# Kernel tuning notes

Hardware: AMD Instinct MI355X
Metric: run time of the kernel (lower is better)

The kernel has to match this reference:

```python
import jax, jax.numpy as jnp
import numpy as np

N, E, G, L, H, DIN = 50000, 800000, 500, 4, 64, 128
EPS = 1e-5


def _gcn(x, W, b, src, dst, n):
    h = x @ W
    loop = jnp.arange(n)
    s = jnp.concatenate([src, loop])
    d = jnp.concatenate([dst, loop])
    deg = jax.ops.segment_sum(jnp.ones(s.shape[0], x.dtype), d, num_segments=n)
    dinv = jax.lax.rsqrt(jnp.maximum(deg, 1.0))  # deg >= 1 due to self loops
    norm = (dinv[s] * dinv[d])[:, None]
    return jax.ops.segment_sum(h[s] * norm, d, num_segments=n) + b


def _g2(x, W, b, src, dst, n, p=2.0):
    # G2 gradient gate: tau = tanh(scatter_mean_over_src(|X_src - X_dst|^p))
    Xc = jax.nn.relu(_gcn(x, W, b, src, dst, n))
    diff = jnp.abs(Xc[src] - Xc[dst]) ** p  # [E, H]
    s = jax.ops.segment_sum(diff, src, num_segments=n)
    cnt = jax.ops.segment_sum(jnp.ones(src.shape[0], x.dtype), src, num_segments=n)
    return jnp.tanh(s / jnp.maximum(cnt, 1.0)[:, None])


def _bn(x, g, b):
    # BatchNorm1d with batch statistics (training-mode normalization)
    m = x.mean(0)
    v = x.var(0)
    return (x - m) * jax.lax.rsqrt(v + EPS) * g + b


def setup_inputs() -> dict:
    key = jax.random.key(0)
    ks = jax.random.split(key, 24)
    sc_in = 1.0 / np.sqrt(DIN)
    sc_h = 1.0 / np.sqrt(H)
    inp = {
        "x": jax.random.normal(ks[0], (N, DIN), jnp.float32),
        "edge_index": jax.random.randint(ks[1], (2, E), 0, N),
        "batch": jnp.sort(jax.random.randint(ks[2], (N,), 0, G)),
        "preW": jax.random.normal(ks[3], (DIN, H), jnp.float32) * sc_in,
        "preb": jnp.zeros((H,), jnp.float32),
        "convW": jax.random.normal(ks[4], (L, H, H), jnp.float32) * sc_h,
        "convb": jnp.zeros((L, H), jnp.float32),
        "ggW": jax.random.normal(ks[5], (L, H, H), jnp.float32) * sc_h,
        "ggb": jnp.zeros((L, H), jnp.float32),
        "lin1W": jax.random.normal(ks[6], (H, H), jnp.float32) * sc_h,
        "lin1b": jnp.zeros((H,), jnp.float32),
        "lin2W": jax.random.normal(ks[7], (H, H), jnp.float32) * sc_h,
        "lin2b": jnp.zeros((H,), jnp.float32),
        "lin3W": jax.random.normal(ks[8], (H, H), jnp.float32) * sc_h,
        "lin3b": jnp.zeros((H,), jnp.float32),
        "lin4W": jax.random.normal(ks[9], (H, 1), jnp.float32) * sc_h,
        "lin4b": jnp.zeros((1,), jnp.float32),
        "bn_g": jnp.ones((H,), jnp.float32),
        "bn_b": jnp.zeros((H,), jnp.float32),
    }
    return inp


def reference(x, edge_index, batch, preW, preb, convW, convb, ggW, ggb,
              lin1W, lin1b, lin2W, lin2b, lin3W, lin3b, lin4W, lin4b,
              bn_g, bn_b):
    src, dst = edge_index[0], edge_index[1]
    # prelinear (dropout disabled / eval)
    x = jax.nn.relu(x @ preW + preb)
    for l in range(L):
        x_ = jax.nn.relu(_gcn(x, convW[l], convb[l], src, dst, N))
        tau = _g2(x, ggW[l], ggb[l], src, dst, N)
        x = (1.0 - tau) * x + tau * x_
    # readout: global add pool per graph -> [G, H]
    h = jax.ops.segment_sum(x, batch, num_segments=G)
    out = jax.nn.relu(_bn(h @ lin1W + lin1b, bn_g, bn_b))
    out = jax.nn.relu(_bn(out @ lin2W + lin2b, bn_g, bn_b))
    out = jax.nn.relu(_bn(out @ lin3W + lin3b, bn_g, bn_b))
    out = out @ lin4W + lin4b  # [G, 1]
    energy = 0.5 * jnp.sum((x[src] - x[dst]) ** 2)  # dirichlet energy of final x
    return (out, out, energy)
```

## Files before the change

kernel.cpp:

```cpp
#include <hip/hip_runtime.h>
#include <hip/hip_bf16.h>


#define N_NODES 50000
#define N_EDGES 800000
#define N_GRAPH 500
#define N_LAYERS 4
#define HDIM 64
#define DDIN 128
#define BN_EPS 1e-5f
#define NEPART 256
#define SC_CHUNK 2048
#define SC_NBLK ((N_NODES + SC_CHUNK - 1) / SC_CHUNK)
#define NPARTS 8
#define PRNG (N_NODES / NPARTS)
#define FILL_BPP 56

typedef __hip_bfloat16 bf16;


__global__ __launch_bounds__(256) void k_degrees(const int* __restrict__ ei,
                                                 int* __restrict__ deg_in,
                                                 int* __restrict__ deg_out) {
  int part = blockIdx.x & (NPARTS - 1);
  int slice = blockIdx.x >> 3;
  int nslice = gridDim.x >> 3;
  int lo = part * PRNG, hi = lo + PRNG;
  int stride = nslice * 256;
  for (int e = slice * 256 + threadIdx.x; e < N_EDGES; e += stride) {
    int s = ei[e], d = ei[N_EDGES + e];
    if (s >= lo && s < hi) atomicAdd(&deg_out[s], 1);
    if (d >= lo && d < hi) atomicAdd(&deg_in[d], 1);
  }
}

__global__ __launch_bounds__(256) void k_scan1(const int* __restrict__ deg_in,
                                               const int* __restrict__ deg_out,
                                               int* __restrict__ rp_dst,
                                               int* __restrict__ rp_src,
                                               int* __restrict__ bsum) {
  int arr = blockIdx.y;
  const int* in = arr ? deg_out : deg_in;
  int* out = arr ? rp_src : rp_dst;
  int base = blockIdx.x * SC_CHUNK + threadIdx.x * 8;
  int v[8];
  int s = 0;
#pragma unroll
  for (int j = 0; j < 8; ++j) {
    int ii = base + j;
    v[j] = (ii < N_NODES) ? in[ii] : 0;
    s += v[j];
  }
  __shared__ int sh[256];
  sh[threadIdx.x] = s;
  __syncthreads();
  for (int off = 1; off < 256; off <<= 1) {
    int t = (threadIdx.x >= off) ? sh[threadIdx.x - off] : 0;
    __syncthreads();
    sh[threadIdx.x] += t;
    __syncthreads();
  }
  int run = sh[threadIdx.x] - s;
#pragma unroll
  for (int j = 0; j < 8; ++j) {
    int ii = base + j;
    if (ii < N_NODES) out[ii] = run;
    run += v[j];
  }
  if (threadIdx.x == 255) bsum[arr * SC_NBLK + blockIdx.x] = sh[255];
}

__global__ __launch_bounds__(64) void k_scan2(const int* __restrict__ bsum,
                                              int* __restrict__ boff,
                                              int* __restrict__ rp_dst,
                                              int* __restrict__ rp_src) {
  int lane = threadIdx.x;
  for (int a = 0; a < 2; ++a) {
    int v = (lane < SC_NBLK) ? bsum[a * SC_NBLK + lane] : 0;
    int incl = v;
    for (int off = 1; off < 64; off <<= 1) {
      int t = __shfl_up(incl, off);
      if (lane >= off) incl += t;
    }
    if (lane < SC_NBLK) boff[a * SC_NBLK + lane] = incl - v;
  }
  if (lane == 0) {
    rp_dst[N_NODES] = N_EDGES;
    rp_src[N_NODES] = N_EDGES;
  }
}

__global__ __launch_bounds__(256) void k_scan3(const int* __restrict__ boff,
                                               int* __restrict__ rp_dst,
                                               int* __restrict__ rp_src,
                                               int* __restrict__ cur_dst,
                                               int* __restrict__ cur_src,
                                               const int* __restrict__ deg_in,
                                               float* __restrict__ dinv) {
  int arr = blockIdx.y;
  int* rp = arr ? rp_src : rp_dst;
  int* cur = arr ? cur_src : cur_dst;
  int off = boff[arr * SC_NBLK + blockIdx.x];
  int base = blockIdx.x * SC_CHUNK + threadIdx.x * 8;
#pragma unroll
  for (int j = 0; j < 8; ++j) {
    int ii = base + j;
    if (ii < N_NODES) {
      int v = rp[ii] + off;
      rp[ii] = v;
      cur[ii] = v;
      if (arr == 0) dinv[ii] = rsqrtf((float)(deg_in[ii] + 1));
    }
  }
}

__global__ __launch_bounds__(256) void k_fill(const int* __restrict__ ei,
                                              int* __restrict__ cur_dst,
                                              int* __restrict__ cur_src,
                                              int* __restrict__ csr_dst,
                                              int* __restrict__ csr_src) {
  int part = blockIdx.x & (NPARTS - 1);
  int slice = blockIdx.x >> 3;
  int nslice = gridDim.x >> 3;
  int lo = part * PRNG, hi = lo + PRNG;
  int stride = nslice * 256;
  for (int e = slice * 256 + threadIdx.x; e < N_EDGES; e += stride) {
    int s = ei[e], d = ei[N_EDGES + e];
    if (d >= lo && d < hi) {
      int q = atomicAdd(&cur_dst[d], 1);
      csr_dst[q] = s;
    }
    if (s >= lo && s < hi) {
      int q = atomicAdd(&cur_src[s], 1);
      csr_src[q] = d;
    }
  }
}


__global__ __launch_bounds__(256) void k_prelin(const float* __restrict__ x0,
                                                const float* __restrict__ W,
                                                const float* __restrict__ b,
                                                float* __restrict__ x) {
  __shared__ float Ws[DDIN * HDIM];
  for (int t = threadIdx.x; t < DDIN * HDIM; t += 256) Ws[t] = W[t];
  __syncthreads();
  int wave = threadIdx.x >> 6, lane = threadIdx.x & 63;
  float bias = b[lane];
  int stride = gridDim.x * 4;
  for (int i = blockIdx.x * 4 + wave; i < N_NODES; i += stride) {
    const float* xr = x0 + (size_t)i * DDIN;
    float xl0 = xr[lane], xl1 = xr[64 + lane];
    float acc = bias;
#pragma unroll
    for (int k = 0; k < 64; ++k) acc = fmaf(__shfl(xl0, k), Ws[k * 64 + lane], acc);
#pragma unroll
    for (int k = 0; k < 64; ++k) acc = fmaf(__shfl(xl1, k), Ws[(64 + k) * 64 + lane], acc);
    x[(size_t)i * HDIM + lane] = fmaxf(acc, 0.f);
  }
}

__global__ __launch_bounds__(256) void k_agg(const float* __restrict__ x,
                                             const int* __restrict__ rp,
                                             const int* __restrict__ csr,
                                             const float* __restrict__ dinv,
                                             float* __restrict__ aggb) {
  int i = (blockIdx.x * 256 + threadIdx.x) >> 6;
  int lane = threadIdx.x & 63;
  if (i >= N_NODES) return;
  int e0 = rp[i], e1 = rp[i + 1];
  float di = dinv[i];
  size_t li = (size_t)i * HDIM + lane;
  float a0 = x[li] * di, a1 = 0.f, a2 = 0.f, a3 = 0.f;
  for (int base = e0; base < e1; base += 64) {
    int m = e1 - base;
    if (m > 64) m = 64;
    int idx = csr[base + (lane < m ? lane : 0)];
    float dv = dinv[idx];
    int k = 0;
    for (; k + 8 <= m; k += 8) {
      int s0 = __shfl(idx, k), s1 = __shfl(idx, k + 1), s2 = __shfl(idx, k + 2),
          s3 = __shfl(idx, k + 3), s4 = __shfl(idx, k + 4), s5 = __shfl(idx, k + 5),
          s6 = __shfl(idx, k + 6), s7 = __shfl(idx, k + 7);
      float w0 = __shfl(dv, k), w1 = __shfl(dv, k + 1), w2 = __shfl(dv, k + 2),
            w3 = __shfl(dv, k + 3), w4 = __shfl(dv, k + 4), w5 = __shfl(dv, k + 5),
            w6 = __shfl(dv, k + 6), w7 = __shfl(dv, k + 7);
      float v0 = x[(size_t)s0 * HDIM + lane], v1 = x[(size_t)s1 * HDIM + lane];
      float v2 = x[(size_t)s2 * HDIM + lane], v3 = x[(size_t)s3 * HDIM + lane];
      float v4 = x[(size_t)s4 * HDIM + lane], v5 = x[(size_t)s5 * HDIM + lane];
      float v6 = x[(size_t)s6 * HDIM + lane], v7 = x[(size_t)s7 * HDIM + lane];
      a0 = fmaf(v0, w0, a0);
      a1 = fmaf(v1, w1, a1);
      a2 = fmaf(v2, w2, a2);
      a3 = fmaf(v3, w3, a3);
      a0 = fmaf(v4, w4, a0);
      a1 = fmaf(v5, w5, a1);
      a2 = fmaf(v6, w6, a2);
      a3 = fmaf(v7, w7, a3);
    }
    for (; k < m; ++k) {
      int s = __shfl(idx, k);
      float w = __shfl(dv, k);
      a0 = fmaf(x[(size_t)s * HDIM + lane], w, a0);
    }
  }
  aggb[li] = (a0 + a1 + a2 + a3) * di;
}

__global__ __launch_bounds__(256) void k_gemm2(const float* __restrict__ agg,
                                               const float* __restrict__ W1,
                                               const float* __restrict__ W2,
                                               const float* __restrict__ b1,
                                               const float* __restrict__ b2,
                                               float* __restrict__ x_,
                                               bf16* __restrict__ Xch) {
  __shared__ float W1s[HDIM * HDIM], W2s[HDIM * HDIM];
  for (int t = threadIdx.x; t < HDIM * HDIM; t += 256) {
    W1s[t] = W1[t];
    W2s[t] = W2[t];
  }
  __syncthreads();
  int wave = threadIdx.x >> 6, lane = threadIdx.x & 63;
  float bb1 = b1[lane], bb2 = b2[lane];
  int stride = gridDim.x * 4;
  for (int i = blockIdx.x * 4 + wave; i < N_NODES; i += stride) {
    size_t li = (size_t)i * HDIM + lane;
    float xl = agg[li];
    float r1 = 0.f, r2 = 0.f;
#pragma unroll
    for (int k = 0; k < 64; ++k) {
      float xv = __shfl(xl, k);
      r1 = fmaf(xv, W1s[k * 64 + lane], r1);
      r2 = fmaf(xv, W2s[k * 64 + lane], r2);
    }
    x_[li] = fmaxf(r1 + bb1, 0.f);
    Xch[li] = __float2bfloat16(fmaxf(r2 + bb2, 0.f));
  }
}

__global__ __launch_bounds__(256) void k_gate(const bf16* __restrict__ Xch,
                                              const float* __restrict__ x_,
                                              const int* __restrict__ rp,
                                              const int* __restrict__ csr,
                                              float* __restrict__ x,
                                              bf16* __restrict__ xh) {
  int i = (blockIdx.x * 256 + threadIdx.x) >> 6;
  int lane = threadIdx.x & 63;
  if (i >= N_NODES) return;
  int e0 = rp[i], e1 = rp[i + 1];
  float xi = __bfloat162float(Xch[(size_t)i * HDIM + lane]);
  float a0 = 0.f, a1 = 0.f, a2 = 0.f, a3 = 0.f;
  for (int base = e0; base < e1; base += 64) {
    int m = e1 - base;
    if (m > 64) m = 64;
    int idx = csr[base + (lane < m ? lane : 0)];
    int k = 0;
    for (; k + 8 <= m; k += 8) {
      int s0 = __shfl(idx, k), s1 = __shfl(idx, k + 1), s2 = __shfl(idx, k + 2),
          s3 = __shfl(idx, k + 3), s4 = __shfl(idx, k + 4), s5 = __shfl(idx, k + 5),
          s6 = __shfl(idx, k + 6), s7 = __shfl(idx, k + 7);
      float v0 = __bfloat162float(Xch[(size_t)s0 * HDIM + lane]);
      float v1 = __bfloat162float(Xch[(size_t)s1 * HDIM + lane]);
      float v2 = __bfloat162float(Xch[(size_t)s2 * HDIM + lane]);
      float v3 = __bfloat162float(Xch[(size_t)s3 * HDIM + lane]);
      float v4 = __bfloat162float(Xch[(size_t)s4 * HDIM + lane]);
      float v5 = __bfloat162float(Xch[(size_t)s5 * HDIM + lane]);
      float v6 = __bfloat162float(Xch[(size_t)s6 * HDIM + lane]);
      float v7 = __bfloat162float(Xch[(size_t)s7 * HDIM + lane]);
      float t0 = xi - v0, t1 = xi - v1, t2 = xi - v2, t3 = xi - v3;
      float t4 = xi - v4, t5 = xi - v5, t6 = xi - v6, t7 = xi - v7;
      a0 = fmaf(t0, t0, a0);
      a1 = fmaf(t1, t1, a1);
      a2 = fmaf(t2, t2, a2);
      a3 = fmaf(t3, t3, a3);
      a0 = fmaf(t4, t4, a0);
      a1 = fmaf(t5, t5, a1);
      a2 = fmaf(t6, t6, a2);
      a3 = fmaf(t7, t7, a3);
    }
    for (; k < m; ++k) {
      int d = __shfl(idx, k);
      float t = xi - __bfloat162float(Xch[(size_t)d * HDIM + lane]);
      a0 = fmaf(t, t, a0);
    }
  }
  int cnt = e1 - e0;
  float tau = tanhf((a0 + a1 + a2 + a3) / (float)(cnt > 0 ? cnt : 1));
  size_t idx = (size_t)i * HDIM + lane;
  float xn = (1.f - tau) * x[idx] + tau * x_[idx];
  x[idx] = xn;
  xh[idx] = __float2bfloat16(xn);
}

__global__ __launch_bounds__(256) void k_epool(const float* __restrict__ x,
                                               const bf16* __restrict__ xh,
                                               const int* __restrict__ rp,
                                               const int* __restrict__ csr,
                                               const int* __restrict__ batch,
                                               float* __restrict__ hpool,
                                               float* __restrict__ epart) {
  int i = (blockIdx.x * 256 + threadIdx.x) >> 6;
  int lane = threadIdx.x & 63;
  if (i >= N_NODES) return;
  size_t li = (size_t)i * HDIM + lane;
  float xi = __bfloat162float(xh[li]);
  int e0 = rp[i], e1 = rp[i + 1];
  float a0 = 0.f, a1 = 0.f, a2 = 0.f, a3 = 0.f;
  for (int base = e0; base < e1; base += 64) {
    int m = e1 - base;
    if (m > 64) m = 64;
    int idx = csr[base + (lane < m ? lane : 0)];
    int k = 0;
    for (; k + 8 <= m; k += 8) {
      int s0 = __shfl(idx, k), s1 = __shfl(idx, k + 1), s2 = __shfl(idx, k + 2),
          s3 = __shfl(idx, k + 3), s4 = __shfl(idx, k + 4), s5 = __shfl(idx, k + 5),
          s6 = __shfl(idx, k + 6), s7 = __shfl(idx, k + 7);
      float v0 = __bfloat162float(xh[(size_t)s0 * HDIM + lane]);
      float v1 = __bfloat162float(xh[(size_t)s1 * HDIM + lane]);
      float v2 = __bfloat162float(xh[(size_t)s2 * HDIM + lane]);
      float v3 = __bfloat162float(xh[(size_t)s3 * HDIM + lane]);
      float v4 = __bfloat162float(xh[(size_t)s4 * HDIM + lane]);
      float v5 = __bfloat162float(xh[(size_t)s5 * HDIM + lane]);
      float v6 = __bfloat162float(xh[(size_t)s6 * HDIM + lane]);
      float v7 = __bfloat162float(xh[(size_t)s7 * HDIM + lane]);
      float t0 = xi - v0, t1 = xi - v1, t2 = xi - v2, t3 = xi - v3;
      float t4 = xi - v4, t5 = xi - v5, t6 = xi - v6, t7 = xi - v7;
      a0 = fmaf(t0, t0, a0);
      a1 = fmaf(t1, t1, a1);
      a2 = fmaf(t2, t2, a2);
      a3 = fmaf(t3, t3, a3);
      a0 = fmaf(t4, t4, a0);
      a1 = fmaf(t5, t5, a1);
      a2 = fmaf(t6, t6, a2);
      a3 = fmaf(t7, t7, a3);
    }
    for (; k < m; ++k) {
      int d = __shfl(idx, k);
      float t = xi - __bfloat162float(xh[(size_t)d * HDIM + lane]);
      a0 = fmaf(t, t, a0);
    }
  }
  int g = batch[i];
  atomicAdd(&hpool[g * HDIM + lane], x[li]);
  float acc = a0 + a1 + a2 + a3;
  acc += __shfl_down(acc, 32);
  acc += __shfl_down(acc, 16);
  acc += __shfl_down(acc, 8);
  acc += __shfl_down(acc, 4);
  acc += __shfl_down(acc, 2);
  acc += __shfl_down(acc, 1);
  if (lane == 0) atomicAdd(&epart[i & (NEPART - 1)], acc);
}

__global__ __launch_bounds__(256) void k_esum(const float* __restrict__ epart,
                                              float* __restrict__ out_e) {
  __shared__ float sh[NEPART];
  int t = threadIdx.x;
  sh[t] = epart[t];
  __syncthreads();
  for (int off = NEPART / 2; off > 0; off >>= 1) {
    if (t < off) sh[t] += sh[t + off];
    __syncthreads();
  }
  if (t == 0) out_e[0] = 0.5f * sh[0];
}


__global__ __launch_bounds__(256) void k_mlpbn(const float* __restrict__ Hin,
                                               const float* __restrict__ W,
                                               const float* __restrict__ b,
                                               const float* __restrict__ g,
                                               const float* __restrict__ bb,
                                               float* __restrict__ Z) {
  int c = blockIdx.x;
  __shared__ float Wc[HDIM];
  __shared__ float red[256];
  if (threadIdx.x < HDIM) Wc[threadIdx.x] = W[threadIdx.x * HDIM + c];
  __syncthreads();
  int r0 = threadIdx.x, r1 = threadIdx.x + 256;
  float bc = b[c];
  float d0 = bc, d1 = bc;
  if (r0 < N_GRAPH) {
    const float* h = Hin + (size_t)r0 * HDIM;
#pragma unroll
    for (int k = 0; k < HDIM; ++k) d0 = fmaf(h[k], Wc[k], d0);
  }
  if (r1 < N_GRAPH) {
    const float* h = Hin + (size_t)r1 * HDIM;
#pragma unroll
    for (int k = 0; k < HDIM; ++k) d1 = fmaf(h[k], Wc[k], d1);
  }
  red[threadIdx.x] = (r0 < N_GRAPH ? d0 : 0.f) + (r1 < N_GRAPH ? d1 : 0.f);
  __syncthreads();
  for (int off = 128; off > 0; off >>= 1) {
    if (threadIdx.x < off) red[threadIdx.x] += red[threadIdx.x + off];
    __syncthreads();
  }
  float mean = red[0] / (float)N_GRAPH;
  __syncthreads();
  float t0 = (r0 < N_GRAPH) ? d0 - mean : 0.f;
  float t1 = (r1 < N_GRAPH) ? d1 - mean : 0.f;
  red[threadIdx.x] = t0 * t0 + t1 * t1;
  __syncthreads();
  for (int off = 128; off > 0; off >>= 1) {
    if (threadIdx.x < off) red[threadIdx.x] += red[threadIdx.x + off];
    __syncthreads();
  }
  float var = red[0] / (float)N_GRAPH;
  float scale = rsqrtf(var + BN_EPS) * g[c];
  float bias = bb[c];
  if (r0 < N_GRAPH) Z[(size_t)r0 * HDIM + c] = fmaxf(fmaf(t0, scale, bias), 0.f);
  if (r1 < N_GRAPH) Z[(size_t)r1 * HDIM + c] = fmaxf(fmaf(t1, scale, bias), 0.f);
}

__global__ __launch_bounds__(256) void k_final(const float* __restrict__ H,
                                               const float* __restrict__ w,
                                               const float* __restrict__ b,
                                               float* __restrict__ out) {
  int r = blockIdx.x * 256 + threadIdx.x;
  if (r >= N_GRAPH) return;
  float acc = b[0];
#pragma unroll
  for (int k = 0; k < 64; ++k) acc = fmaf(H[r * HDIM + k], w[k], acc);
  out[r] = acc;
  out[N_GRAPH + r] = acc;
}


extern "C" void kernel_launch(void* const* d_in, const int* in_sizes, int n_in,
                              void* d_out, int out_size, void* d_ws, size_t ws_size,
                              hipStream_t stream) {
  (void)in_sizes; (void)n_in; (void)out_size; (void)ws_size;
  const float* x0    = (const float*)d_in[0];
  const int*   ei    = (const int*)d_in[1];
  const int*   batch = (const int*)d_in[2];
  const float* preW  = (const float*)d_in[3];
  const float* preb  = (const float*)d_in[4];
  const float* convW = (const float*)d_in[5];
  const float* convb = (const float*)d_in[6];
  const float* ggW   = (const float*)d_in[7];
  const float* ggb   = (const float*)d_in[8];
  const float* lin1W = (const float*)d_in[9];
  const float* lin1b = (const float*)d_in[10];
  const float* lin2W = (const float*)d_in[11];
  const float* lin2b = (const float*)d_in[12];
  const float* lin3W = (const float*)d_in[13];
  const float* lin3b = (const float*)d_in[14];
  const float* lin4W = (const float*)d_in[15];
  const float* lin4b = (const float*)d_in[16];
  const float* bng   = (const float*)d_in[17];
  const float* bnb   = (const float*)d_in[18];
  float* out = (float*)d_out;

  char* ws = (char*)d_ws;
  size_t off = 0;
  auto alloc = [&](size_t bytes) -> void* {
    off = (off + 255) & ~(size_t)255;
    void* p = ws + off;
    off += bytes;
    return p;
  };
  int* deg_in   = (int*)alloc(2ull * N_NODES * 4);
  int* deg_out  = deg_in + N_NODES;
  int* rp_dst   = (int*)alloc((N_NODES + 1) * 4);
  int* rp_src   = (int*)alloc((N_NODES + 1) * 4);
  int* cur_dst  = (int*)alloc((N_NODES + 1) * 4);
  int* cur_src  = (int*)alloc((N_NODES + 1) * 4);
  int* bsum     = (int*)alloc(2 * SC_NBLK * 4);
  int* boff     = (int*)alloc(2 * SC_NBLK * 4);
  int* csr_dst  = (int*)alloc((size_t)N_EDGES * 4);
  int* csr_src  = (int*)alloc((size_t)N_EDGES * 4);
  float* dinv   = (float*)alloc(N_NODES * 4);
  float* x      = (float*)alloc((size_t)N_NODES * HDIM * 4);
  float* aggb   = (float*)alloc((size_t)N_NODES * HDIM * 4);
  float* x_     = (float*)alloc((size_t)N_NODES * HDIM * 4);
  bf16* Xch     = (bf16*)alloc((size_t)N_NODES * HDIM * 2);
  bf16* xh      = (bf16*)alloc((size_t)N_NODES * HDIM * 2);
  float* hpool  = (float*)alloc(N_GRAPH * HDIM * 4);
  float* epart  = (float*)alloc(NEPART * 4);
  float* mlpA   = (float*)alloc(N_GRAPH * HDIM * 4);
  float* mlpB   = (float*)alloc(N_GRAPH * HDIM * 4);

  hipMemsetAsync(deg_in, 0, 2ull * N_NODES * 4, stream);
  hipMemsetAsync(hpool, 0, N_GRAPH * HDIM * 4, stream);
  hipMemsetAsync(epart, 0, NEPART * 4, stream);

  k_degrees<<<NPARTS * FILL_BPP, 256, 0, stream>>>(ei, deg_in, deg_out);
  {
    dim3 g(SC_NBLK, 2);
    k_scan1<<<g, 256, 0, stream>>>(deg_in, deg_out, rp_dst, rp_src, bsum);
    k_scan2<<<1, 64, 0, stream>>>(bsum, boff, rp_dst, rp_src);
    k_scan3<<<g, 256, 0, stream>>>(boff, rp_dst, rp_src, cur_dst, cur_src, deg_in, dinv);
  }
  k_fill<<<NPARTS * FILL_BPP, 256, 0, stream>>>(ei, cur_dst, cur_src, csr_dst, csr_src);

  k_prelin<<<512, 256, 0, stream>>>(x0, preW, preb, x);

  const int gnode = (N_NODES + 3) / 4;
  for (int l = 0; l < N_LAYERS; ++l) {
    k_agg<<<gnode, 256, 0, stream>>>(x, rp_dst, csr_dst, dinv, aggb);
    k_gemm2<<<1024, 256, 0, stream>>>(aggb, convW + l * HDIM * HDIM, ggW + l * HDIM * HDIM,
                                      convb + l * HDIM, ggb + l * HDIM, x_, Xch);
    k_gate<<<gnode, 256, 0, stream>>>(Xch, x_, rp_src, csr_src, x, xh);
  }

  k_epool<<<gnode, 256, 0, stream>>>(x, xh, rp_src, csr_src, batch, hpool, epart);
  k_esum<<<1, NEPART, 0, stream>>>(epart, out + 2 * N_GRAPH);

  k_mlpbn<<<HDIM, 256, 0, stream>>>(hpool, lin1W, lin1b, bng, bnb, mlpA);
  k_mlpbn<<<HDIM, 256, 0, stream>>>(mlpA, lin2W, lin2b, bng, bnb, mlpB);
  k_mlpbn<<<HDIM, 256, 0, stream>>>(mlpB, lin3W, lin3b, bng, bnb, mlpA);
  k_final<<<(N_GRAPH + 255) / 256, 256, 0, stream>>>(mlpA, lin4W, lin4b, out);
}
```

Baseline: 873.6 us.

## Pre-scale node features by dinv and replace atomic pooling with segmented pool kernel

The producers (prelin and gate) now also write a copy of x pre-multiplied by the node's dinv. This lets the aggregation kernel drop the per-edge dinv gather and shuffles and sum plain values. Graph pooling moves out of the energy kernel's per-node atomics into a separate kernel that binary-searches the sorted batch array and reduces each graph's nodes per block. The cost is an extra fp32 N×H write per layer, an extra buffer, and one more launch.

Measured after the change: 879.4 us. No clear change (+0.7%).

```diff
diff --git a/kernel.cpp b/kernel.cpp
--- a/kernel.cpp
+++ b/kernel.cpp
@@ -141,7 +141,9 @@
 __global__ __launch_bounds__(256) void k_prelin(const float* __restrict__ x0,
                                                 const float* __restrict__ W,
                                                 const float* __restrict__ b,
-                                                float* __restrict__ x) {
+                                                const float* __restrict__ dinv,
+                                                float* __restrict__ x,
+                                                float* __restrict__ xs) {
   __shared__ float Ws[DDIN * HDIM];
   for (int t = threadIdx.x; t < DDIN * HDIM; t += 256) Ws[t] = W[t];
   __syncthreads();
@@ -156,11 +158,14 @@
     for (int k = 0; k < 64; ++k) acc = fmaf(__shfl(xl0, k), Ws[k * 64 + lane], acc);
 #pragma unroll
     for (int k = 0; k < 64; ++k) acc = fmaf(__shfl(xl1, k), Ws[(64 + k) * 64 + lane], acc);
-    x[(size_t)i * HDIM + lane] = fmaxf(acc, 0.f);
-  }
-}
-
-__global__ __launch_bounds__(256) void k_agg(const float* __restrict__ x,
+    float xv = fmaxf(acc, 0.f);
+    size_t li = (size_t)i * HDIM + lane;
+    x[li] = xv;
+    xs[li] = xv * dinv[i];
+  }
+}
+
+__global__ __launch_bounds__(256) void k_agg(const float* __restrict__ xs,
                                              const int* __restrict__ rp,
                                              const int* __restrict__ csr,
                                              const float* __restrict__ dinv,
@@ -171,37 +176,32 @@
   int e0 = rp[i], e1 = rp[i + 1];
   float di = dinv[i];
   size_t li = (size_t)i * HDIM + lane;
-  float a0 = x[li] * di, a1 = 0.f, a2 = 0.f, a3 = 0.f;
+  float a0 = xs[li], a1 = 0.f, a2 = 0.f, a3 = 0.f;
   for (int base = e0; base < e1; base += 64) {
     int m = e1 - base;
     if (m > 64) m = 64;
     int idx = csr[base + (lane < m ? lane : 0)];
-    float dv = dinv[idx];
     int k = 0;
     for (; k + 8 <= m; k += 8) {
       int s0 = __shfl(idx, k), s1 = __shfl(idx, k + 1), s2 = __shfl(idx, k + 2),
           s3 = __shfl(idx, k + 3), s4 = __shfl(idx, k + 4), s5 = __shfl(idx, k + 5),
           s6 = __shfl(idx, k + 6), s7 = __shfl(idx, k + 7);
-      float w0 = __shfl(dv, k), w1 = __shfl(dv, k + 1), w2 = __shfl(dv, k + 2),
-            w3 = __shfl(dv, k + 3), w4 = __shfl(dv, k + 4), w5 = __shfl(dv, k + 5),
-            w6 = __shfl(dv, k + 6), w7 = __shfl(dv, k + 7);
-      float v0 = x[(size_t)s0 * HDIM + lane], v1 = x[(size_t)s1 * HDIM + lane];
-      float v2 = x[(size_t)s2 * HDIM + lane], v3 = x[(size_t)s3 * HDIM + lane];
-      float v4 = x[(size_t)s4 * HDIM + lane], v5 = x[(size_t)s5 * HDIM + lane];
-      float v6 = x[(size_t)s6 * HDIM + lane], v7 = x[(size_t)s7 * HDIM + lane];
-      a0 = fmaf(v0, w0, a0);
-      a1 = fmaf(v1, w1, a1);
-      a2 = fmaf(v2, w2, a2);
-      a3 = fmaf(v3, w3, a3);
-      a0 = fmaf(v4, w4, a0);
-      a1 = fmaf(v5, w5, a1);
-      a2 = fmaf(v6, w6, a2);
-      a3 = fmaf(v7, w7, a3);
+      float v0 = xs[(size_t)s0 * HDIM + lane], v1 = xs[(size_t)s1 * HDIM + lane];
+      float v2 = xs[(size_t)s2 * HDIM + lane], v3 = xs[(size_t)s3 * HDIM + lane];
+      float v4 = xs[(size_t)s4 * HDIM + lane], v5 = xs[(size_t)s5 * HDIM + lane];
+      float v6 = xs[(size_t)s6 * HDIM + lane], v7 = xs[(size_t)s7 * HDIM + lane];
+      a0 += v0;
+      a1 += v1;
+      a2 += v2;
+      a3 += v3;
+      a0 += v4;
+      a1 += v5;
+      a2 += v6;
+      a3 += v7;
     }
     for (; k < m; ++k) {
       int s = __shfl(idx, k);
-      float w = __shfl(dv, k);
-      a0 = fmaf(x[(size_t)s * HDIM + lane], w, a0);
+      a0 += xs[(size_t)s * HDIM + lane];
     }
   }
   aggb[li] = (a0 + a1 + a2 + a3) * di;
@@ -242,8 +242,10 @@
                                               const float* __restrict__ x_,
                                               const int* __restrict__ rp,
                                               const int* __restrict__ csr,
+                                              const float* __restrict__ dinv,
                                               float* __restrict__ x,
-                                              bf16* __restrict__ xh) {
+                                              bf16* __restrict__ xh,
+                                              float* __restrict__ xs) {
   int i = (blockIdx.x * 256 + threadIdx.x) >> 6;
   int lane = threadIdx.x & 63;
   if (i >= N_NODES) return;
@@ -290,14 +292,12 @@
   float xn = (1.f - tau) * x[idx] + tau * x_[idx];
   x[idx] = xn;
   xh[idx] = __float2bfloat16(xn);
-}
-
-__global__ __launch_bounds__(256) void k_epool(const float* __restrict__ x,
-                                               const bf16* __restrict__ xh,
+  xs[idx] = xn * dinv[i];
+}
+
+__global__ __launch_bounds__(256) void k_epool(const bf16* __restrict__ xh,
                                                const int* __restrict__ rp,
                                                const int* __restrict__ csr,
-                                               const int* __restrict__ batch,
-                                               float* __restrict__ hpool,
                                                float* __restrict__ epart) {
   int i = (blockIdx.x * 256 + threadIdx.x) >> 6;
   int lane = threadIdx.x & 63;
@@ -340,8 +340,6 @@
       a0 = fmaf(t, t, a0);
     }
   }
-  int g = batch[i];
-  atomicAdd(&hpool[g * HDIM + lane], x[li]);
   float acc = a0 + a1 + a2 + a3;
   acc += __shfl_down(acc, 32);
   acc += __shfl_down(acc, 16);
@@ -363,6 +361,32 @@
     __syncthreads();
   }
   if (t == 0) out_e[0] = 0.5f * sh[0];
+}
+
+__global__ __launch_bounds__(256) void k_pool2(const float* __restrict__ x,
+                                               const int* __restrict__ batch,
+                                               float* __restrict__ hpool) {
+  int g = blockIdx.x;
+  int a = 0, b = N_NODES;
+  while (a < b) {
+    int mid = (a + b) >> 1;
+    if (batch[mid] < g) a = mid + 1; else b = mid;
+  }
+  int lo = a;
+  b = N_NODES;
+  while (a < b) {
+    int mid = (a + b) >> 1;
+    if (batch[mid] < g + 1) a = mid + 1; else b = mid;
+  }
+  int hi = a;
+  int wave = threadIdx.x >> 6, lane = threadIdx.x & 63;
+  float acc = 0.f;
+  for (int i = lo + wave; i < hi; i += 4) acc += x[(size_t)i * HDIM + lane];
+  __shared__ float sh[4][HDIM];
+  sh[wave][lane] = acc;
+  __syncthreads();
+  if (wave == 0)
+    hpool[g * HDIM + lane] = (sh[0][lane] + sh[1][lane]) + (sh[2][lane] + sh[3][lane]);
 }
 
 
@@ -472,6 +496,7 @@
   int* csr_src  = (int*)alloc((size_t)N_EDGES * 4);
   float* dinv   = (float*)alloc(N_NODES * 4);
   float* x      = (float*)alloc((size_t)N_NODES * HDIM * 4);
+  float* xs     = (float*)alloc((size_t)N_NODES * HDIM * 4);
   float* aggb   = (float*)alloc((size_t)N_NODES * HDIM * 4);
   float* x_     = (float*)alloc((size_t)N_NODES * HDIM * 4);
   bf16* Xch     = (bf16*)alloc((size_t)N_NODES * HDIM * 2);
@@ -482,7 +507,6 @@
   float* mlpB   = (float*)alloc(N_GRAPH * HDIM * 4);
 
   hipMemsetAsync(deg_in, 0, 2ull * N_NODES * 4, stream);
-  hipMemsetAsync(hpool, 0, N_GRAPH * HDIM * 4, stream);
   hipMemsetAsync(epart, 0, NEPART * 4, stream);
 
   k_degrees<<<NPARTS * FILL_BPP, 256, 0, stream>>>(ei, deg_in, deg_out);
@@ -494,18 +518,19 @@
   }
   k_fill<<<NPARTS * FILL_BPP, 256, 0, stream>>>(ei, cur_dst, cur_src, csr_dst, csr_src);
 
-  k_prelin<<<512, 256, 0, stream>>>(x0, preW, preb, x);
+  k_prelin<<<512, 256, 0, stream>>>(x0, preW, preb, dinv, x, xs);
 
   const int gnode = (N_NODES + 3) / 4;
   for (int l = 0; l < N_LAYERS; ++l) {
-    k_agg<<<gnode, 256, 0, stream>>>(x, rp_dst, csr_dst, dinv, aggb);
+    k_agg<<<gnode, 256, 0, stream>>>(xs, rp_dst, csr_dst, dinv, aggb);
     k_gemm2<<<1024, 256, 0, stream>>>(aggb, convW + l * HDIM * HDIM, ggW + l * HDIM * HDIM,
                                       convb + l * HDIM, ggb + l * HDIM, x_, Xch);
-    k_gate<<<gnode, 256, 0, stream>>>(Xch, x_, rp_src, csr_src, x, xh);
-  }
-
-  k_epool<<<gnode, 256, 0, stream>>>(x, xh, rp_src, csr_src, batch, hpool, epart);
+    k_gate<<<gnode, 256, 0, stream>>>(Xch, x_, rp_src, csr_src, dinv, x, xh, xs);
+  }
+
+  k_epool<<<gnode, 256, 0, stream>>>(xh, rp_src, csr_src, epart);
   k_esum<<<1, NEPART, 0, stream>>>(epart, out + 2 * N_GRAPH);
+  k_pool2<<<N_GRAPH, 256, 0, stream>>>(x, batch, hpool);
 
   k_mlpbn<<<HDIM, 256, 0, stream>>>(hpool, lin1W, lin1b, bng, bnb, mlpA);
   k_mlpbn<<<HDIM, 256, 0, stream>>>(mlpA, lin2W, lin2b, bng, bnb, mlpB);
```
